# Optimization experiments

Hardware: AMD Instinct MI355X
Metric: run time of the kernel (lower is better)

Reference implementation:

```python
import jax, jax.numpy as jnp
import numpy as np

N_NODES = 50000
N_EDGES = 800000
IN_DIM = 128
HIDDEN = 128
LN_EPS = 1e-5


def setup_inputs() -> dict:
    key = jax.random.key(0)
    ks = jax.random.split(key, 10)
    x = jax.random.normal(ks[0], (N_NODES, IN_DIM), dtype=jnp.float32)
    edge_index = jax.random.randint(ks[1], (2, N_EDGES), 0, N_NODES, dtype=jnp.int32)
    # GCNConv linear weights (glorot-ish) + bias, per layer
    W1 = jax.random.normal(ks[2], (IN_DIM, HIDDEN), dtype=jnp.float32) / np.sqrt(IN_DIM)
    b1 = jnp.zeros((HIDDEN,), dtype=jnp.float32)
    W2 = jax.random.normal(ks[3], (HIDDEN, HIDDEN), dtype=jnp.float32) / np.sqrt(HIDDEN)
    b2 = jnp.zeros((HIDDEN,), dtype=jnp.float32)
    # LayerNorm affine params per layer
    g1 = jnp.ones((HIDDEN,), dtype=jnp.float32)
    beta1 = jnp.zeros((HIDDEN,), dtype=jnp.float32)
    g2 = jnp.ones((HIDDEN,), dtype=jnp.float32)
    beta2 = jnp.zeros((HIDDEN,), dtype=jnp.float32)
    return {"x": x, "edge_index": edge_index, "W1": W1, "b1": b1,
            "g1": g1, "beta1": beta1, "W2": W2, "b2": b2,
            "g2": g2, "beta2": beta2}


def _gcn_layer(h, W, b, src, dst):
    # h: [N, Din] -> [N, Dout]; src/dst: [E] (source j -> target i)
    n = h.shape[0]
    h = h @ W
    loops = jnp.arange(n, dtype=src.dtype)
    s = jnp.concatenate([src, loops])  # [E+N]
    d = jnp.concatenate([dst, loops])
    deg = jax.ops.segment_sum(jnp.ones(s.shape[0], dtype=h.dtype), d, num_segments=n)
    dinv = jnp.where(deg > 0, jax.lax.rsqrt(jnp.maximum(deg, 1.0)), 0.0)
    norm = dinv[s] * dinv[d]  # [E+N] symmetric normalization
    out = jax.ops.segment_sum(h[s] * norm[:, None], d, num_segments=n)
    return out + b


def _layer_norm(h, g, b):
    mu = jnp.mean(h, axis=-1, keepdims=True)
    var = jnp.mean(jnp.square(h - mu), axis=-1, keepdims=True)
    return (h - mu) * jax.lax.rsqrt(var + LN_EPS) * g + b


def reference(x, edge_index, W1, b1, g1, beta1, W2, b2, g2, beta2):
    src, dst = edge_index[0], edge_index[1]
    h = _gcn_layer(x, W1, b1, src, dst)
    h = jax.nn.relu(_layer_norm(h, g1, beta1))
    h = _gcn_layer(h, W2, b2, src, dst)
    h = jax.nn.relu(_layer_norm(h, g2, beta2))
    return h
```

## Files before the change

### kernel.cpp

```cpp
#include <hip/hip_runtime.h>

#define LN_EPS 1e-5f

typedef __attribute__((ext_vector_type(8))) short bf16x8;
typedef __attribute__((ext_vector_type(4))) float f32x4;

#define BSH 7
#define BSPAN 128
#define BCAP 4096
#define BIN_TILE 4096

__device__ __forceinline__ unsigned short f2bf(float f) {
    union { float f; unsigned u; } x; x.f = f;
    unsigned r = (x.u + 0x7FFFu + ((x.u >> 16) & 1u)) >> 16;
    return (unsigned short)r;
}
__device__ __forceinline__ float bfbits2f(unsigned hi) {
    union { unsigned u; float f; } x; x.u = hi; return x.f;
}
__device__ __forceinline__ unsigned cvtpk_bf16(float lo, float hi) {
    unsigned r;
    asm("v_cvt_pk_bf16_f32 %0, %1, %2" : "=v"(r) : "v"(lo), "v"(hi));
    return r;
}

__global__ void packw_k(const float* __restrict__ W1, const float* __restrict__ W2,
                        unsigned short* __restrict__ Wp1, unsigned short* __restrict__ Wp2,
                        int* __restrict__ gcur, int nb) {
    int idx = blockIdx.x * blockDim.x + threadIdx.x;
    if (blockIdx.x == 0) {
        for (int i = threadIdx.x; i < nb; i += 256) gcur[i] = 0;
    }
    const float* W = (idx < 16384) ? W1 : W2;
    unsigned short* Wp = (idx < 16384) ? Wp1 : Wp2;
    int t = idx & 16383;
    int k = t >> 7, col = t & 127;
    int kc = k >> 5, kr = k & 31, kb = kr >> 3, j = kr & 7;
    Wp[(((kc * 128 + col) * 4 + kb) * 8) + j] = f2bf(W[k * 128 + col]);
}

__global__ __launch_bounds__(256) void bin_k(const int* __restrict__ src,
                                             const int* __restrict__ dst,
                                             int* __restrict__ gcur,
                                             unsigned* __restrict__ staging,
                                             int nE, int nb) {
    __shared__ int cnt[512];
    __shared__ int gbase[512];
    int tid = threadIdx.x;
    for (int i = tid; i < nb; i += 256) cnt[i] = 0;
    __syncthreads();
    int e0 = blockIdx.x * BIN_TILE;
    unsigned pk[16];
    int bk[16];
    int rk[16];
#pragma unroll
    for (int i = 0; i < 16; ++i) {
        int e = e0 + i * 256 + tid;
        if (e < nE) {
            int s = src[e];
            int d = dst[e];
            int b = d >> BSH;
            rk[i] = atomicAdd(&cnt[b], 1);
            bk[i] = b;
            pk[i] = (unsigned)s | ((unsigned)(d & (BSPAN - 1)) << 17);
        } else {
            bk[i] = -1;
        }
    }
    __syncthreads();
    for (int i = tid; i < nb; i += 256) gbase[i] = atomicAdd(&gcur[i], cnt[i]);
    __syncthreads();
#pragma unroll
    for (int i = 0; i < 16; ++i) {
        if (bk[i] >= 0)
            staging[(size_t)bk[i] * BCAP + gbase[bk[i]] + rk[i]] = pk[i];
    }
}

__global__ __launch_bounds__(256) void build_k(const unsigned* __restrict__ staging,
                                               const int* __restrict__ gcur,
                                               int* __restrict__ rowptr,
                                               int* __restrict__ eidx,
                                               float* __restrict__ dinv, int n, int nE) {
    __shared__ int cnt[BSPAN];
    __shared__ int off[BSPAN];
    __shared__ int s[BSPAN];
    __shared__ int red[4];
    int b = blockIdx.x;
    int tid = threadIdx.x;
    if (tid < BSPAN) cnt[tid] = 0;
    int part = 0;
    for (int i = tid; i < b; i += 256) part += gcur[i];
#pragma unroll
    for (int o = 32; o > 0; o >>= 1) part += __shfl_down(part, o);
    if ((tid & 63) == 0) red[tid >> 6] = part;
    __syncthreads();
    int base = red[0] + red[1] + red[2] + red[3];
    int total = gcur[b];
    if (b == 0 && tid == 0) rowptr[n] = nE;

    const unsigned* stg = staging + (size_t)b * BCAP;
    unsigned ent[16];
#pragma unroll
    for (int k = 0; k < 16; ++k) {
        int i = tid + k * 256;
        unsigned e = 0xFFFFFFFFu;
        if (i < total) {
            e = stg[i];
            atomicAdd(&cnt[(e >> 17) & (BSPAN - 1)], 1);
        }
        ent[k] = e;
    }
    __syncthreads();
    if (tid < BSPAN) s[tid] = cnt[tid];
    __syncthreads();
    for (int o = 1; o < BSPAN; o <<= 1) {
        int t = (tid < BSPAN && tid >= o) ? s[tid - o] : 0;
        __syncthreads();
        if (tid < BSPAN) s[tid] += t;
        __syncthreads();
    }
    if (tid < BSPAN) {
        int excl = s[tid] - cnt[tid];
        off[tid] = excl;
        int node = b * BSPAN + tid;
        if (node < n) {
            rowptr[node] = base + excl;
            dinv[node] = rsqrtf((float)(cnt[tid] + 1));
        }
    }
    __syncthreads();
#pragma unroll
    for (int k = 0; k < 16; ++k) {
        unsigned e = ent[k];
        if (e != 0xFFFFFFFFu) {
            int ld = (e >> 17) & (BSPAN - 1);
            int p = atomicAdd(&off[ld], 1);
            eidx[base + p] = (int)(e & 0x1FFFFu);
        }
    }
}

template <bool A_F32>
__global__ __launch_bounds__(256) void mfma_gemm_k(const void* __restrict__ Ain,
                                                   const unsigned short* __restrict__ Wp,
                                                   const float* __restrict__ dinv,
                                                   unsigned short* __restrict__ Y, int n) {
    int wid = threadIdx.x >> 6;
    int lane = threadIdx.x & 63;
    int rgrp = wid & 1;
    int cgrp = wid >> 1;
    int row0 = blockIdx.x * 64 + rgrp * 32;
    int m = lane & 15;
    int kb = lane >> 4;

    f32x4 acc[2][4] = {};
#pragma unroll
    for (int kc = 0; kc < 4; ++kc) {
        bf16x8 a[2], b[4];
#pragma unroll
        for (int rs = 0; rs < 2; ++rs) {
            int r = row0 + rs * 16 + m;
            if (A_F32) {
                f32x4 f0 = {0.f, 0.f, 0.f, 0.f}, f1 = {0.f, 0.f, 0.f, 0.f};
                if (r < n) {
                    const float* ap = (const float*)Ain + (size_t)r * 128 + kc * 32 + kb * 8;
                    f0 = *(const f32x4*)ap;
                    f1 = *(const f32x4*)(ap + 4);
                }
                unsigned* w = (unsigned*)&a[rs];
                w[0] = cvtpk_bf16(f0.x, f0.y);
                w[1] = cvtpk_bf16(f0.z, f0.w);
                w[2] = cvtpk_bf16(f1.x, f1.y);
                w[3] = cvtpk_bf16(f1.z, f1.w);
            } else {
                a[rs] = *(const bf16x8*)((const unsigned short*)Ain + (size_t)r * 128 + kc * 32 + kb * 8);
            }
        }
#pragma unroll
        for (int cf = 0; cf < 4; ++cf) {
            int col = cgrp * 64 + cf * 16 + m;
            b[cf] = *(const bf16x8*)(Wp + (((kc * 128 + col) * 4 + kb) * 8));
        }
#pragma unroll
        for (int rs = 0; rs < 2; ++rs)
#pragma unroll
            for (int cf = 0; cf < 4; ++cf)
                acc[rs][cf] = __builtin_amdgcn_mfma_f32_16x16x32_bf16(a[rs], b[cf], acc[rs][cf], 0, 0, 0);
    }
#pragma unroll
    for (int rs = 0; rs < 2; ++rs) {
        int rbase = row0 + rs * 16 + kb * 4;
#pragma unroll
        for (int r = 0; r < 4; ++r) {
            int row = rbase + r;
            if (row >= n) continue;
            float dv = dinv[row];
#pragma unroll
            for (int cf = 0; cf < 4; ++cf) {
                int col = cgrp * 64 + cf * 16 + m;
                Y[(size_t)row * 128 + col] = f2bf(acc[rs][cf][r] * dv);
            }
        }
    }
}

#define ACCS(u, s) { \
    a0 = fmaf(bfbits2f((u).x << 16), s, a0); a1 = fmaf(bfbits2f((u).x & 0xFFFF0000u), s, a1); \
    a2 = fmaf(bfbits2f((u).y << 16), s, a2); a3 = fmaf(bfbits2f((u).y & 0xFFFF0000u), s, a3); \
    a4 = fmaf(bfbits2f((u).z << 16), s, a4); a5 = fmaf(bfbits2f((u).z & 0xFFFF0000u), s, a5); \
    a6 = fmaf(bfbits2f((u).w << 16), s, a6); a7 = fmaf(bfbits2f((u).w & 0xFFFF0000u), s, a7); }

#define GSLOT(EB, OFF, U, S) { \
    int ee = (EB) + (OFF) + grp; \
    bool pp = ee < end; \
    int ec = pp ? ee : (end - 1); \
    int ix = eidx[ec]; \
    int ii = pp ? ix : wave; \
    U = H16[(size_t)ii * 16 + q]; \
    S = pp ? 1.0f : 0.0f; }

template <bool OUT_BF16>
__global__ __launch_bounds__(256) void agg_ln_k(const unsigned short* __restrict__ Hs,
                                                const float* __restrict__ dinv,
                                                const int* __restrict__ rowptr,
                                                const int* __restrict__ eidx,
                                                const float* __restrict__ bias,
                                                const float* __restrict__ g,
                                                const float* __restrict__ beta,
                                                void* __restrict__ out, int n) {
    int wave = (blockIdx.x * blockDim.x + threadIdx.x) >> 6;
    int lane = threadIdx.x & 63;
    if (wave >= n) return;
    int q = lane & 15;
    int grp = lane >> 4;
    const uint4* H16 = (const uint4*)Hs;

    int beg = rowptr[wave];
    int end = rowptr[wave + 1];
    float dt = dinv[wave];

    float a0 = 0.f, a1 = 0.f, a2 = 0.f, a3 = 0.f, a4 = 0.f, a5 = 0.f, a6 = 0.f, a7 = 0.f;
    {
        uint4 sv = H16[(size_t)wave * 16 + q];
        float ss = (grp == 0) ? 1.0f : 0.0f;
        ACCS(sv, ss);
    }
    if (beg < end) {
        uint4 c0, c1, c2, c3;
        float s0, s1, s2, s3;
        GSLOT(beg, 0, c0, s0);
        GSLOT(beg, 4, c1, s1);
        GSLOT(beg, 8, c2, s2);
        GSLOT(beg, 12, c3, s3);
        for (int eb = beg + 16;; eb += 16) {
            bool more = eb < end;
            uint4 n0 = c0, n1 = c0, n2 = c0, n3 = c0;
            float t0 = 0.f, t1 = 0.f, t2 = 0.f, t3 = 0.f;
            if (more) {
                GSLOT(eb, 0, n0, t0);
                GSLOT(eb, 4, n1, t1);
                GSLOT(eb, 8, n2, t2);
                GSLOT(eb, 12, n3, t3);
            }
            ACCS(c0, s0);
            ACCS(c1, s1);
            ACCS(c2, s2);
            ACCS(c3, s3);
            if (!more) break;
            c0 = n0; c1 = n1; c2 = n2; c3 = n3;
            s0 = t0; s1 = t1; s2 = t2; s3 = t3;
        }
    }
    a0 += __shfl_xor(a0, 16); a1 += __shfl_xor(a1, 16);
    a2 += __shfl_xor(a2, 16); a3 += __shfl_xor(a3, 16);
    a4 += __shfl_xor(a4, 16); a5 += __shfl_xor(a5, 16);
    a6 += __shfl_xor(a6, 16); a7 += __shfl_xor(a7, 16);
    a0 += __shfl_xor(a0, 32); a1 += __shfl_xor(a1, 32);
    a2 += __shfl_xor(a2, 32); a3 += __shfl_xor(a3, 32);
    a4 += __shfl_xor(a4, 32); a5 += __shfl_xor(a5, 32);
    a6 += __shfl_xor(a6, 32); a7 += __shfl_xor(a7, 32);

    float4 bi0 = ((const float4*)bias)[2 * q];
    float4 bi1 = ((const float4*)bias)[2 * q + 1];
    float v0 = a0 * dt + bi0.x, v1 = a1 * dt + bi0.y;
    float v2 = a2 * dt + bi0.z, v3 = a3 * dt + bi0.w;
    float v4 = a4 * dt + bi1.x, v5 = a5 * dt + bi1.y;
    float v6 = a6 * dt + bi1.z, v7 = a7 * dt + bi1.w;

    float sum = ((v0 + v1) + (v2 + v3)) + ((v4 + v5) + (v6 + v7));
    sum += __shfl_xor(sum, 1);
    sum += __shfl_xor(sum, 2);
    sum += __shfl_xor(sum, 4);
    sum += __shfl_xor(sum, 8);
    float mu = sum * (1.0f / 128.0f);
    float d0 = v0 - mu, d1 = v1 - mu, d2 = v2 - mu, d3 = v3 - mu;
    float d4 = v4 - mu, d5 = v5 - mu, d6 = v6 - mu, d7 = v7 - mu;
    float vs = ((d0 * d0 + d1 * d1) + (d2 * d2 + d3 * d3)) +
               ((d4 * d4 + d5 * d5) + (d6 * d6 + d7 * d7));
    vs += __shfl_xor(vs, 1);
    vs += __shfl_xor(vs, 2);
    vs += __shfl_xor(vs, 4);
    vs += __shfl_xor(vs, 8);
    float rstd = rsqrtf(vs * (1.0f / 128.0f) + LN_EPS);

    float4 gg0 = ((const float4*)g)[2 * q];
    float4 gg1 = ((const float4*)g)[2 * q + 1];
    float4 bb0 = ((const float4*)beta)[2 * q];
    float4 bb1 = ((const float4*)beta)[2 * q + 1];
    float o0 = fmaxf(d0 * rstd * gg0.x + bb0.x, 0.0f);
    float o1 = fmaxf(d1 * rstd * gg0.y + bb0.y, 0.0f);
    float o2 = fmaxf(d2 * rstd * gg0.z + bb0.z, 0.0f);
    float o3 = fmaxf(d3 * rstd * gg0.w + bb0.w, 0.0f);
    float o4 = fmaxf(d4 * rstd * gg1.x + bb1.x, 0.0f);
    float o5 = fmaxf(d5 * rstd * gg1.y + bb1.y, 0.0f);
    float o6 = fmaxf(d6 * rstd * gg1.z + bb1.z, 0.0f);
    float o7 = fmaxf(d7 * rstd * gg1.w + bb1.w, 0.0f);

    if (grp == 0) {
        if (OUT_BF16) {
            uint4 pk;
            pk.x = (unsigned)f2bf(o0) | ((unsigned)f2bf(o1) << 16);
            pk.y = (unsigned)f2bf(o2) | ((unsigned)f2bf(o3) << 16);
            pk.z = (unsigned)f2bf(o4) | ((unsigned)f2bf(o5) << 16);
            pk.w = (unsigned)f2bf(o6) | ((unsigned)f2bf(o7) << 16);
            ((uint4*)out)[(size_t)wave * 16 + q] = pk;
        } else {
            float4* o = (float4*)out;
            o[(size_t)wave * 32 + 2 * q]     = make_float4(o0, o1, o2, o3);
            o[(size_t)wave * 32 + 2 * q + 1] = make_float4(o4, o5, o6, o7);
        }
    }
}

extern "C" void kernel_launch(void* const* d_in, const int* in_sizes, int n_in,
                              void* d_out, int out_size, void* d_ws, size_t ws_size,
                              hipStream_t stream) {
    const float* x   = (const float*)d_in[0];
    const int*   ei  = (const int*)d_in[1];
    const float* W1  = (const float*)d_in[2];
    const float* b1  = (const float*)d_in[3];
    const float* g1  = (const float*)d_in[4];
    const float* be1 = (const float*)d_in[5];
    const float* W2  = (const float*)d_in[6];
    const float* b2  = (const float*)d_in[7];
    const float* g2  = (const float*)d_in[8];
    const float* be2 = (const float*)d_in[9];
    float* out = (float*)d_out;

    int n  = in_sizes[0] / 128;
    int nE = in_sizes[1] / 2;
    const int* src = ei;
    const int* dst = ei + nE;

    int nb = (n + BSPAN - 1) >> BSH;
    int nblk64 = (n + 63) / 64;
    int npad   = nblk64 * 64;

    char* p = (char*)d_ws;
    auto carve = [&](size_t bytes) {
        char* r = p;
        p += (bytes + 255) & ~(size_t)255;
        return r;
    };
    float*    dinv    = (float*)carve((size_t)n * 4);
    int*      rowptr  = (int*)carve((size_t)(n + 1) * 4);
    int*      eidx    = (int*)carve((size_t)nE * 4);
    int*      gcur    = (int*)carve((size_t)nb * 4);
    unsigned* staging = (unsigned*)carve((size_t)nb * BCAP * 4);
    unsigned short* Wp1 = (unsigned short*)carve(16384 * 2);
    unsigned short* Wp2 = (unsigned short*)carve(16384 * 2);
    unsigned short* Hs  = (unsigned short*)carve((size_t)npad * 128 * 2);
    unsigned short* Hb  = (unsigned short*)carve((size_t)npad * 128 * 2);

    dim3 blk(256);
    int nbin = (nE + BIN_TILE - 1) / BIN_TILE;
    int nwave_blocks = (n + 3) / 4;

    packw_k<<<32768 / 256, blk, 0, stream>>>(W1, W2, Wp1, Wp2, gcur, nb);

    bin_k<<<nbin, blk, 0, stream>>>(src, dst, gcur, staging, nE, nb);
    build_k<<<nb, blk, 0, stream>>>(staging, gcur, rowptr, eidx, dinv, n, nE);

    mfma_gemm_k<true><<<nblk64, blk, 0, stream>>>(x, Wp1, dinv, Hs, n);
    agg_ln_k<true><<<nwave_blocks, blk, 0, stream>>>(Hs, dinv, rowptr, eidx, b1, g1, be1, Hb, n);

    mfma_gemm_k<false><<<nblk64, blk, 0, stream>>>(Hb, Wp2, dinv, Hs, n);
    agg_ln_k<false><<<nwave_blocks, blk, 0, stream>>>(Hs, dinv, rowptr, eidx, b2, g2, be2, out, n);
}
```

Measured before the change: 210.4 us.

## Fuse layer-1 aggregation and LayerNorm with the layer-2 GEMM through an LDS tile

Adds a new kernel in which each 256-thread block aggregates 64 nodes, with each wave walking 16 nodes in turn, and applies bias, LayerNorm and ReLU. It writes the bf16 rows into a padded shared-memory tile, then multiplies that tile by W2 with MFMA and scales by dinv. This drops one kernel launch and the global write and re-read of the intermediate bf16 hidden buffer. The cost is much lower parallelism in the latency-bound gather: 782 blocks of sequential per-wave node loops instead of one wave per node across 12500 blocks. It also adds a block-wide barrier before the GEMM.

```diff
diff --git a/kernel.cpp b/kernel.cpp
--- a/kernel.cpp
+++ b/kernel.cpp
@@ -9,6 +9,7 @@
 #define BSPAN 128
 #define BCAP 4096
 #define BIN_TILE 4096
+#define ASTRIDE 136
 
 __device__ __forceinline__ unsigned short f2bf(float f) {
     union { float f; unsigned u; } x; x.f = f;
@@ -141,8 +142,7 @@
     }
 }
 
-template <bool A_F32>
-__global__ __launch_bounds__(256) void mfma_gemm_k(const void* __restrict__ Ain,
+__global__ __launch_bounds__(256) void mfma_gemm_k(const float* __restrict__ Ain,
                                                    const unsigned short* __restrict__ Wp,
                                                    const float* __restrict__ dinv,
                                                    unsigned short* __restrict__ Y, int n) {
@@ -161,21 +161,17 @@
 #pragma unroll
         for (int rs = 0; rs < 2; ++rs) {
             int r = row0 + rs * 16 + m;
-            if (A_F32) {
-                f32x4 f0 = {0.f, 0.f, 0.f, 0.f}, f1 = {0.f, 0.f, 0.f, 0.f};
-                if (r < n) {
-                    const float* ap = (const float*)Ain + (size_t)r * 128 + kc * 32 + kb * 8;
-                    f0 = *(const f32x4*)ap;
-                    f1 = *(const f32x4*)(ap + 4);
-                }
-                unsigned* w = (unsigned*)&a[rs];
-                w[0] = cvtpk_bf16(f0.x, f0.y);
-                w[1] = cvtpk_bf16(f0.z, f0.w);
-                w[2] = cvtpk_bf16(f1.x, f1.y);
-                w[3] = cvtpk_bf16(f1.z, f1.w);
-            } else {
-                a[rs] = *(const bf16x8*)((const unsigned short*)Ain + (size_t)r * 128 + kc * 32 + kb * 8);
+            f32x4 f0 = {0.f, 0.f, 0.f, 0.f}, f1 = {0.f, 0.f, 0.f, 0.f};
+            if (r < n) {
+                const float* ap = Ain + (size_t)r * 128 + kc * 32 + kb * 8;
+                f0 = *(const f32x4*)ap;
+                f1 = *(const f32x4*)(ap + 4);
             }
+            unsigned* w = (unsigned*)&a[rs];
+            w[0] = cvtpk_bf16(f0.x, f0.y);
+            w[1] = cvtpk_bf16(f0.z, f0.w);
+            w[2] = cvtpk_bf16(f1.x, f1.y);
+            w[3] = cvtpk_bf16(f1.z, f1.w);
         }
 #pragma unroll
         for (int cf = 0; cf < 4; ++cf) {
@@ -220,7 +216,74 @@
     U = H16[(size_t)ii * 16 + q]; \
     S = pp ? 1.0f : 0.0f; }
 
-template <bool OUT_BF16>
+#define AGG_BODY() { \
+    uint4 sv = H16[(size_t)wave * 16 + q]; \
+    float ss = (grp == 0) ? 1.0f : 0.0f; \
+    ACCS(sv, ss); \
+    if (beg < end) { \
+        uint4 c0, c1, c2, c3; \
+        float s0, s1, s2, s3; \
+        GSLOT(beg, 0, c0, s0); \
+        GSLOT(beg, 4, c1, s1); \
+        GSLOT(beg, 8, c2, s2); \
+        GSLOT(beg, 12, c3, s3); \
+        for (int eb = beg + 16;; eb += 16) { \
+            bool more = eb < end; \
+            uint4 n0 = c0, n1 = c0, n2 = c0, n3 = c0; \
+            float t0 = 0.f, t1 = 0.f, t2 = 0.f, t3 = 0.f; \
+            if (more) { \
+                GSLOT(eb, 0, n0, t0); \
+                GSLOT(eb, 4, n1, t1); \
+                GSLOT(eb, 8, n2, t2); \
+                GSLOT(eb, 12, n3, t3); \
+            } \
+            ACCS(c0, s0); \
+            ACCS(c1, s1); \
+            ACCS(c2, s2); \
+            ACCS(c3, s3); \
+            if (!more) break; \
+            c0 = n0; c1 = n1; c2 = n2; c3 = n3; \
+            s0 = t0; s1 = t1; s2 = t2; s3 = t3; \
+        } \
+    } \
+    a0 += __shfl_xor(a0, 16); a1 += __shfl_xor(a1, 16); \
+    a2 += __shfl_xor(a2, 16); a3 += __shfl_xor(a3, 16); \
+    a4 += __shfl_xor(a4, 16); a5 += __shfl_xor(a5, 16); \
+    a6 += __shfl_xor(a6, 16); a7 += __shfl_xor(a7, 16); \
+    a0 += __shfl_xor(a0, 32); a1 += __shfl_xor(a1, 32); \
+    a2 += __shfl_xor(a2, 32); a3 += __shfl_xor(a3, 32); \
+    a4 += __shfl_xor(a4, 32); a5 += __shfl_xor(a5, 32); \
+    a6 += __shfl_xor(a6, 32); a7 += __shfl_xor(a7, 32); }
+
+#define LN_BODY() \
+    float v0 = a0 * dt + bi0.x, v1 = a1 * dt + bi0.y; \
+    float v2 = a2 * dt + bi0.z, v3 = a3 * dt + bi0.w; \
+    float v4 = a4 * dt + bi1.x, v5 = a5 * dt + bi1.y; \
+    float v6 = a6 * dt + bi1.z, v7 = a7 * dt + bi1.w; \
+    float sum = ((v0 + v1) + (v2 + v3)) + ((v4 + v5) + (v6 + v7)); \
+    sum += __shfl_xor(sum, 1); \
+    sum += __shfl_xor(sum, 2); \
+    sum += __shfl_xor(sum, 4); \
+    sum += __shfl_xor(sum, 8); \
+    float mu = sum * (1.0f / 128.0f); \
+    float d0 = v0 - mu, d1 = v1 - mu, d2 = v2 - mu, d3 = v3 - mu; \
+    float d4 = v4 - mu, d5 = v5 - mu, d6 = v6 - mu, d7 = v7 - mu; \
+    float vs = ((d0 * d0 + d1 * d1) + (d2 * d2 + d3 * d3)) + \
+               ((d4 * d4 + d5 * d5) + (d6 * d6 + d7 * d7)); \
+    vs += __shfl_xor(vs, 1); \
+    vs += __shfl_xor(vs, 2); \
+    vs += __shfl_xor(vs, 4); \
+    vs += __shfl_xor(vs, 8); \
+    float rstd = rsqrtf(vs * (1.0f / 128.0f) + LN_EPS); \
+    float o0 = fmaxf(d0 * rstd * gg0.x + bb0.x, 0.0f); \
+    float o1 = fmaxf(d1 * rstd * gg0.y + bb0.y, 0.0f); \
+    float o2 = fmaxf(d2 * rstd * gg0.z + bb0.z, 0.0f); \
+    float o3 = fmaxf(d3 * rstd * gg0.w + bb0.w, 0.0f); \
+    float o4 = fmaxf(d4 * rstd * gg1.x + bb1.x, 0.0f); \
+    float o5 = fmaxf(d5 * rstd * gg1.y + bb1.y, 0.0f); \
+    float o6 = fmaxf(d6 * rstd * gg1.z + bb1.z, 0.0f); \
+    float o7 = fmaxf(d7 * rstd * gg1.w + bb1.w, 0.0f);
+
 __global__ __launch_bounds__(256) void agg_ln_k(const unsigned short* __restrict__ Hs,
                                                 const float* __restrict__ dinv,
                                                 const int* __restrict__ rowptr,
@@ -228,7 +291,7 @@
                                                 const float* __restrict__ bias,
                                                 const float* __restrict__ g,
                                                 const float* __restrict__ beta,
-                                                void* __restrict__ out, int n) {
+                                                float* __restrict__ out, int n) {
     int wave = (blockIdx.x * blockDim.x + threadIdx.x) >> 6;
     int lane = threadIdx.x & 63;
     if (wave >= n) return;
@@ -239,96 +302,105 @@
     int beg = rowptr[wave];
     int end = rowptr[wave + 1];
     float dt = dinv[wave];
-
-    float a0 = 0.f, a1 = 0.f, a2 = 0.f, a3 = 0.f, a4 = 0.f, a5 = 0.f, a6 = 0.f, a7 = 0.f;
-    {
-        uint4 sv = H16[(size_t)wave * 16 + q];
-        float ss = (grp == 0) ? 1.0f : 0.0f;
-        ACCS(sv, ss);
-    }
-    if (beg < end) {
-        uint4 c0, c1, c2, c3;
-        float s0, s1, s2, s3;
-        GSLOT(beg, 0, c0, s0);
-        GSLOT(beg, 4, c1, s1);
-        GSLOT(beg, 8, c2, s2);
-        GSLOT(beg, 12, c3, s3);
-        for (int eb = beg + 16;; eb += 16) {
-            bool more = eb < end;
-            uint4 n0 = c0, n1 = c0, n2 = c0, n3 = c0;
-            float t0 = 0.f, t1 = 0.f, t2 = 0.f, t3 = 0.f;
-            if (more) {
-                GSLOT(eb, 0, n0, t0);
-                GSLOT(eb, 4, n1, t1);
-                GSLOT(eb, 8, n2, t2);
-                GSLOT(eb, 12, n3, t3);
-            }
-            ACCS(c0, s0);
-            ACCS(c1, s1);
-            ACCS(c2, s2);
-            ACCS(c3, s3);
-            if (!more) break;
-            c0 = n0; c1 = n1; c2 = n2; c3 = n3;
-            s0 = t0; s1 = t1; s2 = t2; s3 = t3;
-        }
-    }
-    a0 += __shfl_xor(a0, 16); a1 += __shfl_xor(a1, 16);
-    a2 += __shfl_xor(a2, 16); a3 += __shfl_xor(a3, 16);
-    a4 += __shfl_xor(a4, 16); a5 += __shfl_xor(a5, 16);
-    a6 += __shfl_xor(a6, 16); a7 += __shfl_xor(a7, 16);
-    a0 += __shfl_xor(a0, 32); a1 += __shfl_xor(a1, 32);
-    a2 += __shfl_xor(a2, 32); a3 += __shfl_xor(a3, 32);
-    a4 += __shfl_xor(a4, 32); a5 += __shfl_xor(a5, 32);
-    a6 += __shfl_xor(a6, 32); a7 += __shfl_xor(a7, 32);
-
     float4 bi0 = ((const float4*)bias)[2 * q];
     float4 bi1 = ((const float4*)bias)[2 * q + 1];
-    float v0 = a0 * dt + bi0.x, v1 = a1 * dt + bi0.y;
-    float v2 = a2 * dt + bi0.z, v3 = a3 * dt + bi0.w;
-    float v4 = a4 * dt + bi1.x, v5 = a5 * dt + bi1.y;
-    float v6 = a6 * dt + bi1.z, v7 = a7 * dt + bi1.w;
-
-    float sum = ((v0 + v1) + (v2 + v3)) + ((v4 + v5) + (v6 + v7));
-    sum += __shfl_xor(sum, 1);
-    sum += __shfl_xor(sum, 2);
-    sum += __shfl_xor(sum, 4);
-    sum += __shfl_xor(sum, 8);
-    float mu = sum * (1.0f / 128.0f);
-    float d0 = v0 - mu, d1 = v1 - mu, d2 = v2 - mu, d3 = v3 - mu;
-    float d4 = v4 - mu, d5 = v5 - mu, d6 = v6 - mu, d7 = v7 - mu;
-    float vs = ((d0 * d0 + d1 * d1) + (d2 * d2 + d3 * d3)) +
-               ((d4 * d4 + d5 * d5) + (d6 * d6 + d7 * d7));
-    vs += __shfl_xor(vs, 1);
-    vs += __shfl_xor(vs, 2);
-    vs += __shfl_xor(vs, 4);
-    vs += __shfl_xor(vs, 8);
-    float rstd = rsqrtf(vs * (1.0f / 128.0f) + LN_EPS);
-
     float4 gg0 = ((const float4*)g)[2 * q];
     float4 gg1 = ((const float4*)g)[2 * q + 1];
     float4 bb0 = ((const float4*)beta)[2 * q];
     float4 bb1 = ((const float4*)beta)[2 * q + 1];
-    float o0 = fmaxf(d0 * rstd * gg0.x + bb0.x, 0.0f);
-    float o1 = fmaxf(d1 * rstd * gg0.y + bb0.y, 0.0f);
-    float o2 = fmaxf(d2 * rstd * gg0.z + bb0.z, 0.0f);
-    float o3 = fmaxf(d3 * rstd * gg0.w + bb0.w, 0.0f);
-    float o4 = fmaxf(d4 * rstd * gg1.x + bb1.x, 0.0f);
-    float o5 = fmaxf(d5 * rstd * gg1.y + bb1.y, 0.0f);
-    float o6 = fmaxf(d6 * rstd * gg1.z + bb1.z, 0.0f);
-    float o7 = fmaxf(d7 * rstd * gg1.w + bb1.w, 0.0f);
+
+    float a0 = 0.f, a1 = 0.f, a2 = 0.f, a3 = 0.f, a4 = 0.f, a5 = 0.f, a6 = 0.f, a7 = 0.f;
+    AGG_BODY();
+    LN_BODY();
 
     if (grp == 0) {
-        if (OUT_BF16) {
+        float4* o = (float4*)out;
+        o[(size_t)wave * 32 + 2 * q]     = make_float4(o0, o1, o2, o3);
+        o[(size_t)wave * 32 + 2 * q + 1] = make_float4(o4, o5, o6, o7);
+    }
+}
+
+__global__ __launch_bounds__(256) void agg_gemm_k(const unsigned short* __restrict__ Hs,
+                                                  const float* __restrict__ dinv,
+                                                  const int* __restrict__ rowptr,
+                                                  const int* __restrict__ eidx,
+                                                  const float* __restrict__ bias,
+                                                  const float* __restrict__ g,
+                                                  const float* __restrict__ beta,
+                                                  const unsigned short* __restrict__ Wp,
+                                                  unsigned short* __restrict__ Y, int n) {
+    __shared__ unsigned short At[64 * ASTRIDE];
+    int tid = threadIdx.x;
+    int w = tid >> 6;
+    int lane = tid & 63;
+    int q = lane & 15;
+    int grp = lane >> 4;
+    const uint4* H16 = (const uint4*)Hs;
+
+    float4 bi0 = ((const float4*)bias)[2 * q];
+    float4 bi1 = ((const float4*)bias)[2 * q + 1];
+    float4 gg0 = ((const float4*)g)[2 * q];
+    float4 gg1 = ((const float4*)g)[2 * q + 1];
+    float4 bb0 = ((const float4*)beta)[2 * q];
+    float4 bb1 = ((const float4*)beta)[2 * q + 1];
+
+    int node0 = blockIdx.x * 64 + w * 16;
+    for (int i = 0; i < 16; ++i) {
+        int wave = node0 + i;
+        if (wave >= n) break;
+        int beg = rowptr[wave];
+        int end = rowptr[wave + 1];
+        float dt = dinv[wave];
+        float a0 = 0.f, a1 = 0.f, a2 = 0.f, a3 = 0.f, a4 = 0.f, a5 = 0.f, a6 = 0.f, a7 = 0.f;
+        AGG_BODY();
+        LN_BODY();
+        if (grp == 0) {
             uint4 pk;
             pk.x = (unsigned)f2bf(o0) | ((unsigned)f2bf(o1) << 16);
             pk.y = (unsigned)f2bf(o2) | ((unsigned)f2bf(o3) << 16);
             pk.z = (unsigned)f2bf(o4) | ((unsigned)f2bf(o5) << 16);
             pk.w = (unsigned)f2bf(o6) | ((unsigned)f2bf(o7) << 16);
-            ((uint4*)out)[(size_t)wave * 16 + q] = pk;
-        } else {
-            float4* o = (float4*)out;
-            o[(size_t)wave * 32 + 2 * q]     = make_float4(o0, o1, o2, o3);
-            o[(size_t)wave * 32 + 2 * q + 1] = make_float4(o4, o5, o6, o7);
+            *(uint4*)(At + (size_t)(w * 16 + i) * ASTRIDE + q * 8) = pk;
+        }
+    }
+    __syncthreads();
+
+    int rgrp = w & 1;
+    int cgrp = w >> 1;
+    int m = q;
+    int kb = grp;
+    f32x4 acc[2][4] = {};
+#pragma unroll
+    for (int kc = 0; kc < 4; ++kc) {
+        bf16x8 a[2], b[4];
+#pragma unroll
+        for (int rs = 0; rs < 2; ++rs)
+            a[rs] = *(const bf16x8*)(At + (size_t)(rgrp * 32 + rs * 16 + m) * ASTRIDE + kc * 32 + kb * 8);
+#pragma unroll
+        for (int cf = 0; cf < 4; ++cf) {
+            int col = cgrp * 64 + cf * 16 + m;
+            b[cf] = *(const bf16x8*)(Wp + (((kc * 128 + col) * 4 + kb) * 8));
+        }
+#pragma unroll
+        for (int rs = 0; rs < 2; ++rs)
+#pragma unroll
+            for (int cf = 0; cf < 4; ++cf)
+                acc[rs][cf] = __builtin_amdgcn_mfma_f32_16x16x32_bf16(a[rs], b[cf], acc[rs][cf], 0, 0, 0);
+    }
+    int row00 = blockIdx.x * 64 + rgrp * 32;
+#pragma unroll
+    for (int rs = 0; rs < 2; ++rs) {
+        int rbase = row00 + rs * 16 + kb * 4;
+#pragma unroll
+        for (int r = 0; r < 4; ++r) {
+            int row = rbase + r;
+            if (row >= n) continue;
+            float dv = dinv[row];
+#pragma unroll
+            for (int cf = 0; cf < 4; ++cf) {
+                int col = cgrp * 64 + cf * 16 + m;
+                Y[(size_t)row * 128 + col] = f2bf(acc[rs][cf][r] * dv);
+            }
         }
     }
 }
@@ -371,7 +443,7 @@
     unsigned short* Wp1 = (unsigned short*)carve(16384 * 2);
     unsigned short* Wp2 = (unsigned short*)carve(16384 * 2);
     unsigned short* Hs  = (unsigned short*)carve((size_t)npad * 128 * 2);
-    unsigned short* Hb  = (unsigned short*)carve((size_t)npad * 128 * 2);
+    unsigned short* Hs2 = (unsigned short*)carve((size_t)npad * 128 * 2);
 
     dim3 blk(256);
     int nbin = (nE + BIN_TILE - 1) / BIN_TILE;
@@ -382,9 +454,9 @@
     bin_k<<<nbin, blk, 0, stream>>>(src, dst, gcur, staging, nE, nb);
     build_k<<<nb, blk, 0, stream>>>(staging, gcur, rowptr, eidx, dinv, n, nE);
 
-    mfma_gemm_k<true><<<nblk64, blk, 0, stream>>>(x, Wp1, dinv, Hs, n);
-    agg_ln_k<true><<<nwave_blocks, blk, 0, stream>>>(Hs, dinv, rowptr, eidx, b1, g1, be1, Hb, n);
-
-    mfma_gemm_k<false><<<nblk64, blk, 0, stream>>>(Hb, Wp2, dinv, Hs, n);
-    agg_ln_k<false><<<nwave_blocks, blk, 0, stream>>>(Hs, dinv, rowptr, eidx, b2, g2, be2, out, n);
-}
+    mfma_gemm_k<<<nblk64, blk, 0, stream>>>(x, Wp1, dinv, Hs, n);
+
+    agg_gemm_k<<<nblk64, blk, 0, stream>>>(Hs, dinv, rowptr, eidx, b1, g1, be1, Wp2, Hs2, n);
+
+    agg_ln_k<<<nwave_blocks, blk, 0, stream>>>(Hs2, dinv, rowptr, eidx, b2, g2, be2, out, n);
+}
```

Result: slower. 246.9 us (+17.4%).

## Fuse weight packing, edge binning and CSR build into one cooperative kernel

Applied to the files above, without the earlier changes.

Merges the three preprocessing kernels (weight pack plus counter reset, edge binning, per-bucket CSR build) into a single cooperative launch that uses grid-wide syncs between phases. Weight packing runs on extra blocks in parallel with binning. The aim is to remove two kernel launch boundaries and their drain/refill gaps. In exchange, every block must be co-resident for the cooperative launch, and grid.sync has its own cost. With nb≈391 and nbin≈196+128 this is about 391 blocks, which should fit on the device.

```diff
diff --git a/kernel.cpp b/kernel.cpp
--- a/kernel.cpp
+++ b/kernel.cpp
@@ -1,4 +1,7 @@
 #include <hip/hip_runtime.h>
+#include <hip/hip_cooperative_groups.h>
+
+namespace cg = cooperative_groups;
 
 #define LN_EPS 1e-5f
 
@@ -24,70 +27,73 @@
     return r;
 }
 
-__global__ void packw_k(const float* __restrict__ W1, const float* __restrict__ W2,
-                        unsigned short* __restrict__ Wp1, unsigned short* __restrict__ Wp2,
-                        int* __restrict__ gcur, int nb) {
-    int idx = blockIdx.x * blockDim.x + threadIdx.x;
-    if (blockIdx.x == 0) {
-        for (int i = threadIdx.x; i < nb; i += 256) gcur[i] = 0;
-    }
-    const float* W = (idx < 16384) ? W1 : W2;
-    unsigned short* Wp = (idx < 16384) ? Wp1 : Wp2;
-    int t = idx & 16383;
-    int k = t >> 7, col = t & 127;
-    int kc = k >> 5, kr = k & 31, kb = kr >> 3, j = kr & 7;
-    Wp[(((kc * 128 + col) * 4 + kb) * 8) + j] = f2bf(W[k * 128 + col]);
-}
-
-__global__ __launch_bounds__(256) void bin_k(const int* __restrict__ src,
-                                             const int* __restrict__ dst,
-                                             int* __restrict__ gcur,
-                                             unsigned* __restrict__ staging,
-                                             int nE, int nb) {
-    __shared__ int cnt[512];
+__global__ __launch_bounds__(256) void csr_coop_k(const int* __restrict__ src,
+                                                  const int* __restrict__ dst,
+                                                  int* __restrict__ gcur,
+                                                  unsigned* __restrict__ staging,
+                                                  const float* __restrict__ W1,
+                                                  const float* __restrict__ W2,
+                                                  unsigned short* __restrict__ Wp1,
+                                                  unsigned short* __restrict__ Wp2,
+                                                  int* __restrict__ rowptr,
+                                                  int* __restrict__ eidx,
+                                                  float* __restrict__ dinv,
+                                                  int n, int nE, int nb, int nbin) {
+    cg::grid_group grid = cg::this_grid();
+    int b = blockIdx.x;
+    int tid = threadIdx.x;
+
+    __shared__ int bcnt[512];
     __shared__ int gbase[512];
-    int tid = threadIdx.x;
-    for (int i = tid; i < nb; i += 256) cnt[i] = 0;
-    __syncthreads();
-    int e0 = blockIdx.x * BIN_TILE;
-    unsigned pk[16];
-    int bk[16];
-    int rk[16];
-#pragma unroll
-    for (int i = 0; i < 16; ++i) {
-        int e = e0 + i * 256 + tid;
-        if (e < nE) {
-            int s = src[e];
-            int d = dst[e];
-            int b = d >> BSH;
-            rk[i] = atomicAdd(&cnt[b], 1);
-            bk[i] = b;
-            pk[i] = (unsigned)s | ((unsigned)(d & (BSPAN - 1)) << 17);
-        } else {
-            bk[i] = -1;
-        }
-    }
-    __syncthreads();
-    for (int i = tid; i < nb; i += 256) gbase[i] = atomicAdd(&gcur[i], cnt[i]);
-    __syncthreads();
-#pragma unroll
-    for (int i = 0; i < 16; ++i) {
-        if (bk[i] >= 0)
-            staging[(size_t)bk[i] * BCAP + gbase[bk[i]] + rk[i]] = pk[i];
-    }
-}
-
-__global__ __launch_bounds__(256) void build_k(const unsigned* __restrict__ staging,
-                                               const int* __restrict__ gcur,
-                                               int* __restrict__ rowptr,
-                                               int* __restrict__ eidx,
-                                               float* __restrict__ dinv, int n, int nE) {
     __shared__ int cnt[BSPAN];
     __shared__ int off[BSPAN];
     __shared__ int s[BSPAN];
     __shared__ int red[4];
-    int b = blockIdx.x;
-    int tid = threadIdx.x;
+
+    if (tid == 0 && b < nb) gcur[b] = 0;
+    grid.sync();
+
+    if (b < nbin) {
+        for (int i = tid; i < nb; i += 256) bcnt[i] = 0;
+        __syncthreads();
+        int e0 = b * BIN_TILE;
+        unsigned pk[16];
+        int bk[16];
+        int rk[16];
+#pragma unroll
+        for (int i = 0; i < 16; ++i) {
+            int e = e0 + i * 256 + tid;
+            if (e < nE) {
+                int sv = src[e];
+                int d = dst[e];
+                int bb = d >> BSH;
+                rk[i] = atomicAdd(&bcnt[bb], 1);
+                bk[i] = bb;
+                pk[i] = (unsigned)sv | ((unsigned)(d & (BSPAN - 1)) << 17);
+            } else {
+                bk[i] = -1;
+            }
+        }
+        __syncthreads();
+        for (int i = tid; i < nb; i += 256) gbase[i] = atomicAdd(&gcur[i], bcnt[i]);
+        __syncthreads();
+#pragma unroll
+        for (int i = 0; i < 16; ++i) {
+            if (bk[i] >= 0)
+                staging[(size_t)bk[i] * BCAP + gbase[bk[i]] + rk[i]] = pk[i];
+        }
+    } else if (b < nbin + 128) {
+        int idx = (b - nbin) * 256 + tid;
+        const float* W = (idx < 16384) ? W1 : W2;
+        unsigned short* Wp = (idx < 16384) ? Wp1 : Wp2;
+        int t = idx & 16383;
+        int k = t >> 7, col = t & 127;
+        int kc = k >> 5, kr = k & 31, kb = kr >> 3, j = kr & 7;
+        Wp[(((kc * 128 + col) * 4 + kb) * 8) + j] = f2bf(W[k * 128 + col]);
+    }
+    grid.sync();
+
+    if (b >= nb) return;
     if (tid < BSPAN) cnt[tid] = 0;
     int part = 0;
     for (int i = tid; i < b; i += 256) part += gcur[i];
@@ -376,11 +382,15 @@
     dim3 blk(256);
     int nbin = (nE + BIN_TILE - 1) / BIN_TILE;
     int nwave_blocks = (n + 3) / 4;
-
-    packw_k<<<32768 / 256, blk, 0, stream>>>(W1, W2, Wp1, Wp2, gcur, nb);
-
-    bin_k<<<nbin, blk, 0, stream>>>(src, dst, gcur, staging, nE, nb);
-    build_k<<<nb, blk, 0, stream>>>(staging, gcur, rowptr, eidx, dinv, n, nE);
+    int ncoop = (nb > nbin + 128) ? nb : (nbin + 128);
+
+    {
+        void* args[] = {(void*)&src, (void*)&dst, (void*)&gcur, (void*)&staging,
+                        (void*)&W1, (void*)&W2, (void*)&Wp1, (void*)&Wp2,
+                        (void*)&rowptr, (void*)&eidx, (void*)&dinv,
+                        (void*)&n, (void*)&nE, (void*)&nb, (void*)&nbin};
+        hipLaunchCooperativeKernel((const void*)csr_coop_k, dim3(ncoop), blk, args, 0, stream);
+    }
 
     mfma_gemm_k<true><<<nblk64, blk, 0, stream>>>(x, Wp1, dinv, Hs, n);
     agg_ln_k<true><<<nwave_blocks, blk, 0, stream>>>(Hs, dinv, rowptr, eidx, b1, g1, be1, Hb, n);
```

After: 307.9 us. +46.4%, slower.

## Store hidden features in column-segment layout and aggregate segment by segment

Applied to the files above, without the earlier changes.

The bf16 hidden features are stored as four 32-column segments, each laid out contiguously over all nodes. The GEMM writes this layout and the aggregation kernel gathers one segment at a time, with 16 edges per wave and 4 lanes per 64-byte row chunk. Block-wide barriers between segments keep the waves of a block in step. The aim is better L2/MALL locality for random gathers, since each pass touches only a quarter of the feature array. In exchange each wave re-reads its edge indices four times, adds barriers, and does more shuffle reductions.

```diff
diff --git a/kernel.cpp b/kernel.cpp
--- a/kernel.cpp
+++ b/kernel.cpp
@@ -145,7 +145,8 @@
 __global__ __launch_bounds__(256) void mfma_gemm_k(const void* __restrict__ Ain,
                                                    const unsigned short* __restrict__ Wp,
                                                    const float* __restrict__ dinv,
-                                                   unsigned short* __restrict__ Y, int n) {
+                                                   unsigned short* __restrict__ Y,
+                                                   int n, int npad) {
     int wid = threadIdx.x >> 6;
     int lane = threadIdx.x & 63;
     int rgrp = wid & 1;
@@ -174,7 +175,8 @@
                 w[2] = cvtpk_bf16(f1.x, f1.y);
                 w[3] = cvtpk_bf16(f1.z, f1.w);
             } else {
-                a[rs] = *(const bf16x8*)((const unsigned short*)Ain + (size_t)r * 128 + kc * 32 + kb * 8);
+                a[rs] = *(const bf16x8*)((const unsigned short*)Ain +
+                                         ((size_t)kc * npad + r) * 32 + kb * 8);
             }
         }
 #pragma unroll
@@ -199,7 +201,7 @@
 #pragma unroll
             for (int cf = 0; cf < 4; ++cf) {
                 int col = cgrp * 64 + cf * 16 + m;
-                Y[(size_t)row * 128 + col] = f2bf(acc[rs][cf][r] * dv);
+                Y[((size_t)(col >> 5) * npad + row) * 32 + (col & 31)] = f2bf(acc[rs][cf][r] * dv);
             }
         }
     }
@@ -211,13 +213,13 @@
     a4 = fmaf(bfbits2f((u).z << 16), s, a4); a5 = fmaf(bfbits2f((u).z & 0xFFFF0000u), s, a5); \
     a6 = fmaf(bfbits2f((u).w << 16), s, a6); a7 = fmaf(bfbits2f((u).w & 0xFFFF0000u), s, a7); }
 
-#define GSLOT(EB, OFF, U, S) { \
-    int ee = (EB) + (OFF) + grp; \
+#define GS16(EB, U, S) { \
+    int ee = (EB) + eslot; \
     bool pp = ee < end; \
     int ec = pp ? ee : (end - 1); \
     int ix = eidx[ec]; \
-    int ii = pp ? ix : wave; \
-    U = H16[(size_t)ii * 16 + q]; \
+    size_t ii = (size_t)(pp ? ix : node); \
+    U = Hseg[segbase + ii * 4 + l]; \
     S = pp ? 1.0f : 0.0f; }
 
 template <bool OUT_BF16>
@@ -228,65 +230,79 @@
                                                 const float* __restrict__ bias,
                                                 const float* __restrict__ g,
                                                 const float* __restrict__ beta,
-                                                void* __restrict__ out, int n) {
+                                                void* __restrict__ out, int n, int npad) {
     int wave = (blockIdx.x * blockDim.x + threadIdx.x) >> 6;
     int lane = threadIdx.x & 63;
-    if (wave >= n) return;
-    int q = lane & 15;
-    int grp = lane >> 4;
-    const uint4* H16 = (const uint4*)Hs;
-
-    int beg = rowptr[wave];
-    int end = rowptr[wave + 1];
-    float dt = dinv[wave];
-
-    float a0 = 0.f, a1 = 0.f, a2 = 0.f, a3 = 0.f, a4 = 0.f, a5 = 0.f, a6 = 0.f, a7 = 0.f;
-    {
-        uint4 sv = H16[(size_t)wave * 16 + q];
-        float ss = (grp == 0) ? 1.0f : 0.0f;
-        ACCS(sv, ss);
-    }
-    if (beg < end) {
-        uint4 c0, c1, c2, c3;
-        float s0, s1, s2, s3;
-        GSLOT(beg, 0, c0, s0);
-        GSLOT(beg, 4, c1, s1);
-        GSLOT(beg, 8, c2, s2);
-        GSLOT(beg, 12, c3, s3);
-        for (int eb = beg + 16;; eb += 16) {
-            bool more = eb < end;
-            uint4 n0 = c0, n1 = c0, n2 = c0, n3 = c0;
-            float t0 = 0.f, t1 = 0.f, t2 = 0.f, t3 = 0.f;
-            if (more) {
-                GSLOT(eb, 0, n0, t0);
-                GSLOT(eb, 4, n1, t1);
-                GSLOT(eb, 8, n2, t2);
-                GSLOT(eb, 12, n3, t3);
+    int node = (wave < n) ? wave : (n - 1);
+    int eslot = lane >> 2;
+    int l = lane & 3;
+    const uint4* Hseg = (const uint4*)Hs;
+
+    int beg = rowptr[node];
+    int end = rowptr[node + 1];
+    float dt = dinv[node];
+
+    float r0 = 0.f, r1 = 0.f, r2 = 0.f, r3 = 0.f, r4 = 0.f, r5 = 0.f, r6 = 0.f, r7 = 0.f;
+    int myseg = (lane >> 2) & 3;
+#pragma unroll
+    for (int k = 0; k < 4; ++k) {
+        size_t segbase = (size_t)k * npad * 4;
+        float a0 = 0.f, a1 = 0.f, a2 = 0.f, a3 = 0.f, a4 = 0.f, a5 = 0.f, a6 = 0.f, a7 = 0.f;
+        {
+            uint4 sv = Hseg[segbase + (size_t)node * 4 + l];
+            float ss = (eslot == 0) ? 1.0f : 0.0f;
+            ACCS(sv, ss);
+        }
+        if (beg < end) {
+            uint4 c0, c1;
+            float s0, s1;
+            GS16(beg, c0, s0);
+            GS16(beg + 16, c1, s1);
+            for (int eb = beg + 32;; eb += 32) {
+                bool more = eb < end;
+                uint4 n0 = c0, n1 = c0;
+                float t0 = 0.f, t1 = 0.f;
+                if (more) {
+                    GS16(eb, n0, t0);
+                    GS16(eb + 16, n1, t1);
+                }
+                ACCS(c0, s0);
+                ACCS(c1, s1);
+                if (!more) break;
+                c0 = n0; c1 = n1;
+                s0 = t0; s1 = t1;
             }
-            ACCS(c0, s0);
-            ACCS(c1, s1);
-            ACCS(c2, s2);
-            ACCS(c3, s3);
-            if (!more) break;
-            c0 = n0; c1 = n1; c2 = n2; c3 = n3;
-            s0 = t0; s1 = t1; s2 = t2; s3 = t3;
-        }
-    }
-    a0 += __shfl_xor(a0, 16); a1 += __shfl_xor(a1, 16);
-    a2 += __shfl_xor(a2, 16); a3 += __shfl_xor(a3, 16);
-    a4 += __shfl_xor(a4, 16); a5 += __shfl_xor(a5, 16);
-    a6 += __shfl_xor(a6, 16); a7 += __shfl_xor(a7, 16);
-    a0 += __shfl_xor(a0, 32); a1 += __shfl_xor(a1, 32);
-    a2 += __shfl_xor(a2, 32); a3 += __shfl_xor(a3, 32);
-    a4 += __shfl_xor(a4, 32); a5 += __shfl_xor(a5, 32);
-    a6 += __shfl_xor(a6, 32); a7 += __shfl_xor(a7, 32);
-
-    float4 bi0 = ((const float4*)bias)[2 * q];
-    float4 bi1 = ((const float4*)bias)[2 * q + 1];
-    float v0 = a0 * dt + bi0.x, v1 = a1 * dt + bi0.y;
-    float v2 = a2 * dt + bi0.z, v3 = a3 * dt + bi0.w;
-    float v4 = a4 * dt + bi1.x, v5 = a5 * dt + bi1.y;
-    float v6 = a6 * dt + bi1.z, v7 = a7 * dt + bi1.w;
+        }
+        a0 += __shfl_xor(a0, 4);  a1 += __shfl_xor(a1, 4);
+        a2 += __shfl_xor(a2, 4);  a3 += __shfl_xor(a3, 4);
+        a4 += __shfl_xor(a4, 4);  a5 += __shfl_xor(a5, 4);
+        a6 += __shfl_xor(a6, 4);  a7 += __shfl_xor(a7, 4);
+        a0 += __shfl_xor(a0, 8);  a1 += __shfl_xor(a1, 8);
+        a2 += __shfl_xor(a2, 8);  a3 += __shfl_xor(a3, 8);
+        a4 += __shfl_xor(a4, 8);  a5 += __shfl_xor(a5, 8);
+        a6 += __shfl_xor(a6, 8);  a7 += __shfl_xor(a7, 8);
+        a0 += __shfl_xor(a0, 16); a1 += __shfl_xor(a1, 16);
+        a2 += __shfl_xor(a2, 16); a3 += __shfl_xor(a3, 16);
+        a4 += __shfl_xor(a4, 16); a5 += __shfl_xor(a5, 16);
+        a6 += __shfl_xor(a6, 16); a7 += __shfl_xor(a7, 16);
+        a0 += __shfl_xor(a0, 32); a1 += __shfl_xor(a1, 32);
+        a2 += __shfl_xor(a2, 32); a3 += __shfl_xor(a3, 32);
+        a4 += __shfl_xor(a4, 32); a5 += __shfl_xor(a5, 32);
+        a6 += __shfl_xor(a6, 32); a7 += __shfl_xor(a7, 32);
+        if (myseg == k) {
+            r0 = a0; r1 = a1; r2 = a2; r3 = a3;
+            r4 = a4; r5 = a5; r6 = a6; r7 = a7;
+        }
+        if (k < 3) __syncthreads();
+    }
+
+    int db4 = myseg * 8 + l * 2;
+    float4 bi0 = ((const float4*)bias)[db4];
+    float4 bi1 = ((const float4*)bias)[db4 + 1];
+    float v0 = r0 * dt + bi0.x, v1 = r1 * dt + bi0.y;
+    float v2 = r2 * dt + bi0.z, v3 = r3 * dt + bi0.w;
+    float v4 = r4 * dt + bi1.x, v5 = r5 * dt + bi1.y;
+    float v6 = r6 * dt + bi1.z, v7 = r7 * dt + bi1.w;
 
     float sum = ((v0 + v1) + (v2 + v3)) + ((v4 + v5) + (v6 + v7));
     sum += __shfl_xor(sum, 1);
@@ -304,10 +320,10 @@
     vs += __shfl_xor(vs, 8);
     float rstd = rsqrtf(vs * (1.0f / 128.0f) + LN_EPS);
 
-    float4 gg0 = ((const float4*)g)[2 * q];
-    float4 gg1 = ((const float4*)g)[2 * q + 1];
-    float4 bb0 = ((const float4*)beta)[2 * q];
-    float4 bb1 = ((const float4*)beta)[2 * q + 1];
+    float4 gg0 = ((const float4*)g)[db4];
+    float4 gg1 = ((const float4*)g)[db4 + 1];
+    float4 bb0 = ((const float4*)beta)[db4];
+    float4 bb1 = ((const float4*)beta)[db4 + 1];
     float o0 = fmaxf(d0 * rstd * gg0.x + bb0.x, 0.0f);
     float o1 = fmaxf(d1 * rstd * gg0.y + bb0.y, 0.0f);
     float o2 = fmaxf(d2 * rstd * gg0.z + bb0.z, 0.0f);
@@ -317,18 +333,18 @@
     float o6 = fmaxf(d6 * rstd * gg1.z + bb1.z, 0.0f);
     float o7 = fmaxf(d7 * rstd * gg1.w + bb1.w, 0.0f);
 
-    if (grp == 0) {
+    if (wave < n && lane < 16) {
         if (OUT_BF16) {
             uint4 pk;
             pk.x = (unsigned)f2bf(o0) | ((unsigned)f2bf(o1) << 16);
             pk.y = (unsigned)f2bf(o2) | ((unsigned)f2bf(o3) << 16);
             pk.z = (unsigned)f2bf(o4) | ((unsigned)f2bf(o5) << 16);
             pk.w = (unsigned)f2bf(o6) | ((unsigned)f2bf(o7) << 16);
-            ((uint4*)out)[(size_t)wave * 16 + q] = pk;
+            ((uint4*)out)[((size_t)myseg * npad + wave) * 4 + l] = pk;
         } else {
             float4* o = (float4*)out;
-            o[(size_t)wave * 32 + 2 * q]     = make_float4(o0, o1, o2, o3);
-            o[(size_t)wave * 32 + 2 * q + 1] = make_float4(o4, o5, o6, o7);
+            o[(size_t)wave * 32 + db4]     = make_float4(o0, o1, o2, o3);
+            o[(size_t)wave * 32 + db4 + 1] = make_float4(o4, o5, o6, o7);
         }
     }
 }
@@ -382,9 +398,9 @@
     bin_k<<<nbin, blk, 0, stream>>>(src, dst, gcur, staging, nE, nb);
     build_k<<<nb, blk, 0, stream>>>(staging, gcur, rowptr, eidx, dinv, n, nE);
 
-    mfma_gemm_k<true><<<nblk64, blk, 0, stream>>>(x, Wp1, dinv, Hs, n);
-    agg_ln_k<true><<<nwave_blocks, blk, 0, stream>>>(Hs, dinv, rowptr, eidx, b1, g1, be1, Hb, n);
-
-    mfma_gemm_k<false><<<nblk64, blk, 0, stream>>>(Hb, Wp2, dinv, Hs, n);
-    agg_ln_k<false><<<nwave_blocks, blk, 0, stream>>>(Hs, dinv, rowptr, eidx, b2, g2, be2, out, n);
-}
+    mfma_gemm_k<true><<<nblk64, blk, 0, stream>>>(x, Wp1, dinv, Hs, n, npad);
+    agg_ln_k<true><<<nwave_blocks, blk, 0, stream>>>(Hs, dinv, rowptr, eidx, b1, g1, be1, Hb, n, npad);
+
+    mfma_gemm_k<false><<<nblk64, blk, 0, stream>>>(Hb, Wp2, dinv, Hs, n, npad);
+    agg_ln_k<false><<<nwave_blocks, blk, 0, stream>>>(Hs, dinv, rowptr, eidx, b2, g2, be2, out, n, npad);
+}
```

After: 297.5 us. +41.4%, slower.
